# Kernel tuning notes

Measured on AMD Instinct MI355X. Metric: run time of the kernel, lower is better.

## Reference

```python
import jax, jax.numpy as jnp
import numpy as np

D_MODEL = 1024
NUM_HEADS = 16


def setup_inputs() -> dict:
    key = jax.random.key(0)
    ks = jax.random.split(key, 11)
    B, T, D = 4, 2048, D_MODEL
    scale = 1.0 / np.sqrt(D)
    inp = {
        'q': jax.random.normal(ks[0], (B, T, D), jnp.float32),
        'k': jax.random.normal(ks[1], (B, T, D), jnp.float32),
        'v': jax.random.normal(ks[2], (B, T, D), jnp.float32),
        'W_q': jax.random.normal(ks[3], (D, D), jnp.float32) * scale,
        'b_q': jnp.zeros((D,), jnp.float32),
        'W_k': jax.random.normal(ks[4], (D, D), jnp.float32) * scale,
        'b_k': jnp.zeros((D,), jnp.float32),
        'W_v': jax.random.normal(ks[5], (D, D), jnp.float32) * scale,
        'b_v': jnp.zeros((D,), jnp.float32),
        'W_o': jax.random.normal(ks[6], (D, D), jnp.float32) * scale,
        'b_o': jnp.zeros((D,), jnp.float32),
    }
    return inp


def reference(q, k, v, W_q, b_q, W_k, b_k, W_v, b_v, W_o, b_o):
    B, T, D = q.shape
    H = NUM_HEADS
    hd = D // H  # head dim

    def split_heads(x):  # [B,T,D] -> [B,H,T,hd]
        return x.reshape(B, T, H, hd).transpose(0, 2, 1, 3)

    qh = split_heads(q @ W_q + b_q)
    kh = split_heads(k @ W_k + b_k)
    vh = split_heads(v @ W_v + b_v)

    score = jnp.einsum('bhqd,bhkd->bhqk', qh, kh) / jnp.sqrt(jnp.float32(hd))
    attn = jax.nn.softmax(score, axis=-1)
    out = jnp.einsum('bhqk,bhkd->bhqd', attn, vh)  # [B,H,T,hd]
    out = out.transpose(0, 2, 1, 3).reshape(B, T, D)
    return out @ W_o + b_o
```

## Files before the change

kernel.cpp:

```cpp
#include <hip/hip_runtime.h>

typedef __attribute__((ext_vector_type(8))) short s8v;
typedef __attribute__((ext_vector_type(4))) float f4v;
typedef __attribute__((ext_vector_type(16))) float f16v;
typedef __attribute__((ext_vector_type(8))) unsigned short u8v;
typedef __attribute__((ext_vector_type(4))) unsigned short u16x4;
typedef __attribute__((ext_vector_type(4))) unsigned int uint4v;

#define B_ 4
#define T_ 2048
#define D_ 1024
#define H_ 16
#define HD_ 64

__device__ __forceinline__ unsigned short f2bf(float f) {
  unsigned int u = __builtin_bit_cast(unsigned int, f);
  u += 0x7fffu + ((u >> 16) & 1u);
  return (unsigned short)(u >> 16);
}

__device__ __forceinline__ unsigned int packbf2(float lo, float hi) {
  unsigned int u0 = __builtin_bit_cast(unsigned int, lo) + 0x8000u;
  unsigned int u1 = __builtin_bit_cast(unsigned int, hi) + 0x8000u;
  return __builtin_amdgcn_perm(u1, u0, 0x07060302u);
}

__device__ __forceinline__ void gload_lds16(const void* g, void* l) {
  __builtin_amdgcn_global_load_lds(
      (const __attribute__((address_space(1))) unsigned int*)g,
      (__attribute__((address_space(3))) unsigned int*)l, 16, 0, 0);
}

__global__ __launch_bounds__(256) void wt_cvt(
    const float* __restrict__ Wq, const float* __restrict__ Wk,
    const float* __restrict__ Wv, const float* __restrict__ Wo,
    unsigned short* __restrict__ Tq, unsigned short* __restrict__ Tk,
    unsigned short* __restrict__ Tv, unsigned short* __restrict__ To) {
  __shared__ unsigned short tile[32][33];
  int z = blockIdx.z;
  const float* W = (z == 0) ? Wq : (z == 1) ? Wk : (z == 2) ? Wv : Wo;
  unsigned short* Wt = (z == 0) ? Tq : (z == 1) ? Tk : (z == 2) ? Tv : To;
  int k0 = blockIdx.x * 32, n0 = blockIdx.y * 32;
  int t = threadIdx.x;
  int r = t >> 3, c = (t & 7) * 4;
  float4 v = *(const float4*)(W + (size_t)(k0 + r) * D_ + n0 + c);
  tile[r][c + 0] = f2bf(v.x);
  tile[r][c + 1] = f2bf(v.y);
  tile[r][c + 2] = f2bf(v.z);
  tile[r][c + 3] = f2bf(v.w);
  __syncthreads();
  u16x4 o;
  o[0] = tile[c + 0][r];
  o[1] = tile[c + 1][r];
  o[2] = tile[c + 2][r];
  o[3] = tile[c + 3][r];
  *(u16x4*)(Wt + (size_t)(n0 + r) * D_ + k0 + c) = o;
}

__global__ __launch_bounds__(256) void repack_k(const unsigned short* __restrict__ Kp,
                                                unsigned short* __restrict__ Kf) {
  unsigned int g = blockIdx.x * 256 + threadIdx.x;
  unsigned int bh = g >> 14;
  unsigned int r = g & 16383;
  unsigned int c32 = r >> 8;
  unsigned int ks = (r >> 6) & 3;
  unsigned int l2 = r & 63;
  unsigned int l = l2 >> 1, hh = l2 & 1;
  unsigned int b = bh >> 4, h = bh & 15;
  size_t row = (size_t)b * T_ + c32 * 32 + l;
  u8v v = *(const u8v*)(Kp + row * D_ + h * HD_ + ks * 16 + hh * 8);
  *(u8v*)(Kf + (size_t)g * 8) = v;
}

__global__ __launch_bounds__(256) void repack_v(const unsigned short* __restrict__ Vp,
                                                unsigned short* __restrict__ Vf) {
  __shared__ unsigned short tl[64][72];
  unsigned int c64 = blockIdx.x;
  unsigned int bh = blockIdx.y;
  unsigned int b = bh >> 4, h = bh & 15;
  int tid = threadIdx.x;
#pragma unroll
  for (int i = 0; i < 2; i++) {
    int s = i * 256 + tid;
    int row = s >> 3, cir = s & 7;
    u8v v = *(const u8v*)(Vp + ((size_t)(b * T_ + c64 * 64 + row)) * D_ + h * HD_ + cir * 8);
    *(u8v*)&tl[row][cir * 8] = v;
  }
  __syncthreads();
#pragma unroll
  for (int i = 0; i < 2; i++) {
    int s = i * 256 + tid;
    int mdkk = s >> 6;
    int l2 = s & 63;
    int l = l2 >> 1, hh = l2 & 1;
    int md = mdkk >> 2, kk = mdkk & 3;
    u8v o;
#pragma unroll
    for (int j = 0; j < 8; j++) o[j] = tl[kk * 16 + hh * 8 + j][md * 32 + l];
    *(u8v*)(Vf + ((size_t)(bh * 32 + c64) * 8 + mdkk) * 512 + l2 * 8) = o;
  }
}

struct GemmArgs {
  const void* A[3];
  const unsigned short* B[3];
  const float* bias[3];
  void* C[3];
};

template <bool AF32, bool OUTF32>
__global__ __launch_bounds__(256) void gemm128(GemmArgs args, int M, int N, int K) {
  __shared__ unsigned char smem[(AF32 ? 16384 : 8192) + 8192];
  unsigned char* AsB = smem;
  unsigned char* BsB = smem + (AF32 ? 16384 : 8192);
  int z = blockIdx.z;
  const float* Af = (const float*)args.A[z];
  const unsigned short* Ab = (const unsigned short*)args.A[z];
  const unsigned short* Bt = args.B[z];
  const float* bias = args.bias[z];
  int tid = threadIdx.x;
  int wave = tid >> 6, lane = tid & 63;
  int dl = lane & 15, quad = lane >> 4;
  int wm = (wave >> 1) * 64, wn = (wave & 1) * 64;
  size_t m0 = (size_t)blockIdx.y * 128, n0 = (size_t)blockIdx.x * 128;
  f4v acc[4][4] = {};

  for (int k0 = 0; k0 < K; k0 += 32) {
    if constexpr (AF32) {
#pragma unroll
      for (int i = 0; i < 4; i++) {
        int s = i * 256 + tid;
        int row = s >> 3, cs = s & 7, csrc = cs ^ (row & 7);
        gload_lds16(Af + (m0 + row) * K + k0 + csrc * 4, AsB + s * 16);
      }
    } else {
#pragma unroll
      for (int i = 0; i < 2; i++) {
        int s = i * 256 + tid;
        int row = s >> 2, cs = s & 3, csrc = cs ^ ((row >> 1) & 3);
        gload_lds16(Ab + (m0 + row) * K + k0 + csrc * 8, AsB + s * 16);
      }
    }
#pragma unroll
    for (int i = 0; i < 2; i++) {
      int s = i * 256 + tid;
      int row = s >> 2, cs = s & 3, csrc = cs ^ ((row >> 1) & 3);
      gload_lds16(Bt + (n0 + row) * K + k0 + csrc * 8, BsB + s * 16);
    }
    __syncthreads();
    s8v af[4], bf4[4];
#pragma unroll
    for (int i = 0; i < 4; i++) {
      int row = wm + i * 16 + dl;
      if constexpr (AF32) {
        const float* Ar = (const float*)AsB + row * 32;
        int f = row & 7;
        float4 lo = *(const float4*)(Ar + ((2 * quad) ^ f) * 4);
        float4 hi = *(const float4*)(Ar + ((2 * quad + 1) ^ f) * 4);
        uint4v p;
        p[0] = packbf2(lo.x, lo.y);
        p[1] = packbf2(lo.z, lo.w);
        p[2] = packbf2(hi.x, hi.y);
        p[3] = packbf2(hi.z, hi.w);
        af[i] = __builtin_bit_cast(s8v, p);
      } else {
        const unsigned short* Ar = (const unsigned short*)AsB + row * 32;
        af[i] = *(const s8v*)(Ar + (quad ^ ((row >> 1) & 3)) * 8);
      }
    }
#pragma unroll
    for (int i = 0; i < 4; i++) {
      int row = wn + i * 16 + dl;
      const unsigned short* Br = (const unsigned short*)BsB + row * 32;
      bf4[i] = *(const s8v*)(Br + (quad ^ ((row >> 1) & 3)) * 8);
    }
#pragma unroll
    for (int mi = 0; mi < 4; mi++)
#pragma unroll
      for (int ni = 0; ni < 4; ni++)
        acc[mi][ni] = __builtin_amdgcn_mfma_f32_16x16x32_bf16(af[mi], bf4[ni], acc[mi][ni], 0, 0, 0);
    __syncthreads();
  }

#pragma unroll
  for (int ni = 0; ni < 4; ni++) {
    size_t col = n0 + wn + ni * 16 + dl;
    float bv = bias[col];
#pragma unroll
    for (int mi = 0; mi < 4; mi++) {
#pragma unroll
      for (int r = 0; r < 4; r++) {
        size_t row = m0 + wm + mi * 16 + quad * 4 + r;
        float v = acc[mi][ni][r] + bv;
        if constexpr (OUTF32) ((float*)args.C[z])[row * N + col] = v;
        else ((unsigned short*)args.C[z])[row * N + col] = f2bf(v);
      }
    }
  }
}

__global__ __launch_bounds__(256) void attn(
    const unsigned short* __restrict__ Q, const unsigned short* __restrict__ Kf,
    const unsigned short* __restrict__ Vf, unsigned short* __restrict__ Ctx) {
  int tid = threadIdx.x;
  int wave = tid >> 6, lane = tid & 63;
  int l31 = lane & 31, hh = lane >> 5;
  int b = blockIdx.z, h = blockIdx.y;
  int bh = b * H_ + h;
  int qbase = blockIdx.x * 128 + wave * 32;
  const unsigned short* Qb = Q + ((size_t)(b * T_ + qbase + l31)) * D_ + h * HD_;
  const unsigned short* Kfb = Kf + (size_t)bh * (T_ * HD_);
  const unsigned short* Vfb = Vf + (size_t)bh * (T_ * HD_);
  int lc = (l31 * 2 + hh) * 8;

  s8v qf[4];
#pragma unroll
  for (int ks = 0; ks < 4; ks++) qf[ks] = *(const s8v*)(Qb + ks * 16 + 8 * hh);

  f16v zero = {};
  f16v oacc[2] = {zero, zero};
  float l = 0.f;
  const float sc = 0.18033688011112042f;

  s8v kf[2][2][4];
#pragma unroll
  for (int ms = 0; ms < 2; ms++)
#pragma unroll
    for (int ks = 0; ks < 4; ks++)
      kf[0][ms][ks] = *(const s8v*)(Kfb + (size_t)(ms * 4 + ks) * 512 + lc);

#pragma unroll 2
  for (int it = 0; it < T_ / 64; ++it) {
    int kt = it * 64;
    int cur = it & 1, nxt = cur ^ 1;
    s8v vf[2][4];
#pragma unroll
    for (int md = 0; md < 2; md++)
#pragma unroll
      for (int kk = 0; kk < 4; kk++)
        vf[md][kk] = *(const s8v*)(Vfb + ((size_t)(kt >> 6) * 8 + md * 4 + kk) * 512 + lc);
    int ktn = (kt + 64) & (T_ - 1);
#pragma unroll
    for (int ms = 0; ms < 2; ms++)
#pragma unroll
      for (int ks = 0; ks < 4; ks++)
        kf[nxt][ms][ks] = *(const s8v*)(Kfb + ((size_t)((ktn >> 5) + ms) * 4 + ks) * 512 + lc);

    f16v sacc[2] = {zero, zero};
#pragma unroll
    for (int ks = 0; ks < 4; ks++)
#pragma unroll
      for (int ms = 0; ms < 2; ms++)
        sacc[ms] = __builtin_amdgcn_mfma_f32_32x32x16_bf16(kf[cur][ms][ks], qf[ks], sacc[ms], 0, 0, 0);

    unsigned int pk[2][8];
#pragma unroll
    for (int ms = 0; ms < 2; ms++)
#pragma unroll
      for (int i = 0; i < 8; i++) {
        float p0 = exp2f(__builtin_fmaf(sacc[ms][2 * i], sc, -16.f));
        float p1 = exp2f(__builtin_fmaf(sacc[ms][2 * i + 1], sc, -16.f));
        l += p0 + p1;
        pk[ms][i] = packbf2(p0, p1);
      }

#pragma unroll
    for (int kk = 0; kk < 4; kk++) {
      int ms = kk >> 1, e4 = (kk & 1) * 4;
      unsigned int y0 = __shfl_xor(pk[ms][e4 + 2], 32);
      unsigned int y1 = __shfl_xor(pk[ms][e4 + 3], 32);
      unsigned int y2 = __shfl_xor(pk[ms][e4 + 0], 32);
      unsigned int y3 = __shfl_xor(pk[ms][e4 + 1], 32);
      uint4v pd;
      pd[0] = hh ? y0 : pk[ms][e4 + 0];
      pd[1] = hh ? y1 : pk[ms][e4 + 1];
      pd[2] = hh ? pk[ms][e4 + 2] : y2;
      pd[3] = hh ? pk[ms][e4 + 3] : y3;
      s8v pf = __builtin_bit_cast(s8v, pd);
#pragma unroll
      for (int md = 0; md < 2; md++)
        oacc[md] = __builtin_amdgcn_mfma_f32_32x32x16_bf16(vf[md][kk], pf, oacc[md], 0, 0, 0);
    }
  }

  l += __shfl_xor(l, 32);
  float inv = 1.0f / l;
  unsigned short* crow = Ctx + ((size_t)(b * T_ + qbase + l31)) * D_ + h * HD_;
#pragma unroll
  for (int md = 0; md < 2; md++)
#pragma unroll
    for (int hi = 0; hi < 4; hi++) {
      unsigned int w0 = packbf2(oacc[md][hi * 4 + 0] * inv, oacc[md][hi * 4 + 1] * inv);
      unsigned int w1 = packbf2(oacc[md][hi * 4 + 2] * inv, oacc[md][hi * 4 + 3] * inv);
      unsigned int* dst = (unsigned int*)(crow + md * 32 + hi * 8 + 4 * hh);
      dst[0] = w0;
      dst[1] = w1;
    }
}

extern "C" void kernel_launch(void* const* d_in, const int* in_sizes, int n_in,
                              void* d_out, int out_size, void* d_ws, size_t ws_size,
                              hipStream_t stream) {
  const float* q = (const float*)d_in[0];
  const float* k = (const float*)d_in[1];
  const float* v = (const float*)d_in[2];
  const float* Wq = (const float*)d_in[3];
  const float* bq = (const float*)d_in[4];
  const float* Wk = (const float*)d_in[5];
  const float* bk = (const float*)d_in[6];
  const float* Wv = (const float*)d_in[7];
  const float* bv = (const float*)d_in[8];
  const float* Wo = (const float*)d_in[9];
  const float* bo = (const float*)d_in[10];
  float* out = (float*)d_out;

  char* ws = (char*)d_ws;
  const size_t MB = 1ull << 20;
  unsigned short* Tq = (unsigned short*)(ws + 0 * MB);
  unsigned short* Tk = (unsigned short*)(ws + 2 * MB);
  unsigned short* Tv = (unsigned short*)(ws + 4 * MB);
  unsigned short* To = (unsigned short*)(ws + 6 * MB);
  unsigned short* Qp = (unsigned short*)(ws + 8 * MB);
  unsigned short* Kp = (unsigned short*)(ws + 24 * MB);
  unsigned short* Vp = (unsigned short*)(ws + 40 * MB);
  unsigned short* Kf = (unsigned short*)(ws + 56 * MB);
  unsigned short* Vf = (unsigned short*)(ws + 72 * MB);
  unsigned short* Ctx = Kp;
  const int M = B_ * T_;

  wt_cvt<<<dim3(32, 32, 4), 256, 0, stream>>>(Wq, Wk, Wv, Wo, Tq, Tk, Tv, To);

  GemmArgs ga;
  ga.A[0] = q;  ga.A[1] = k;  ga.A[2] = v;
  ga.B[0] = Tq; ga.B[1] = Tk; ga.B[2] = Tv;
  ga.bias[0] = bq; ga.bias[1] = bk; ga.bias[2] = bv;
  ga.C[0] = Qp; ga.C[1] = Kp; ga.C[2] = Vp;
  gemm128<true, false><<<dim3(D_ / 128, M / 128, 3), 256, 0, stream>>>(ga, M, D_, D_);

  repack_k<<<dim3(4096), 256, 0, stream>>>(Kp, Kf);
  repack_v<<<dim3(32, 64), 256, 0, stream>>>(Vp, Vf);

  attn<<<dim3(T_ / 128, H_, B_), 256, 0, stream>>>(Qp, Kf, Vf, Ctx);

  GemmArgs go;
  go.A[0] = Ctx; go.B[0] = To; go.bias[0] = bo; go.C[0] = out;
  gemm128<false, true><<<dim3(D_ / 128, M / 128, 1), 256, 0, stream>>>(go, M, D_, D_);
}
```

Before: 515.4 us.

## Reshape QKV GEMM wave tiling and remap attention blocks for XCD locality

The fp32-input QKV projection GEMM now gives each wave a 32x128 tile instead of 64x64. Each wave converts fewer fp32 A rows to bf16, in exchange for more B fragment loads per wave. The attention kernel now launches single-wave blocks on a flat grid of 4096. Block IDs are remapped so that all query blocks of one (batch, head) land on the same XCD, aiming for better L2 reuse of K/V. Smaller blocks may change occupancy and scheduling overhead.

```diff
diff --git a/kernel.cpp b/kernel.cpp
--- a/kernel.cpp
+++ b/kernel.cpp
@@ -110,6 +110,8 @@
 
 template <bool AF32, bool OUTF32>
 __global__ __launch_bounds__(256) void gemm128(GemmArgs args, int M, int N, int K) {
+  constexpr int MI = AF32 ? 2 : 4;
+  constexpr int NI = AF32 ? 8 : 4;
   __shared__ unsigned char smem[(AF32 ? 16384 : 8192) + 8192];
   unsigned char* AsB = smem;
   unsigned char* BsB = smem + (AF32 ? 16384 : 8192);
@@ -121,9 +123,10 @@
   int tid = threadIdx.x;
   int wave = tid >> 6, lane = tid & 63;
   int dl = lane & 15, quad = lane >> 4;
-  int wm = (wave >> 1) * 64, wn = (wave & 1) * 64;
+  int wm = AF32 ? wave * 32 : (wave >> 1) * 64;
+  int wn = AF32 ? 0 : (wave & 1) * 64;
   size_t m0 = (size_t)blockIdx.y * 128, n0 = (size_t)blockIdx.x * 128;
-  f4v acc[4][4] = {};
+  f4v acc[MI][NI] = {};
 
   for (int k0 = 0; k0 < K; k0 += 32) {
     if constexpr (AF32) {
@@ -148,9 +151,9 @@
       gload_lds16(Bt + (n0 + row) * K + k0 + csrc * 8, BsB + s * 16);
     }
     __syncthreads();
-    s8v af[4], bf4[4];
-#pragma unroll
-    for (int i = 0; i < 4; i++) {
+    s8v af[MI], bf4[NI];
+#pragma unroll
+    for (int i = 0; i < MI; i++) {
       int row = wm + i * 16 + dl;
       if constexpr (AF32) {
         const float* Ar = (const float*)AsB + row * 32;
@@ -169,25 +172,25 @@
       }
     }
 #pragma unroll
-    for (int i = 0; i < 4; i++) {
+    for (int i = 0; i < NI; i++) {
       int row = wn + i * 16 + dl;
       const unsigned short* Br = (const unsigned short*)BsB + row * 32;
       bf4[i] = *(const s8v*)(Br + (quad ^ ((row >> 1) & 3)) * 8);
     }
 #pragma unroll
-    for (int mi = 0; mi < 4; mi++)
-#pragma unroll
-      for (int ni = 0; ni < 4; ni++)
+    for (int mi = 0; mi < MI; mi++)
+#pragma unroll
+      for (int ni = 0; ni < NI; ni++)
         acc[mi][ni] = __builtin_amdgcn_mfma_f32_16x16x32_bf16(af[mi], bf4[ni], acc[mi][ni], 0, 0, 0);
     __syncthreads();
   }
 
 #pragma unroll
-  for (int ni = 0; ni < 4; ni++) {
+  for (int ni = 0; ni < NI; ni++) {
     size_t col = n0 + wn + ni * 16 + dl;
     float bv = bias[col];
 #pragma unroll
-    for (int mi = 0; mi < 4; mi++) {
+    for (int mi = 0; mi < MI; mi++) {
 #pragma unroll
       for (int r = 0; r < 4; r++) {
         size_t row = m0 + wm + mi * 16 + quad * 4 + r;
@@ -199,15 +202,17 @@
   }
 }
 
-__global__ __launch_bounds__(256) void attn(
+__global__ __launch_bounds__(64) void attn(
     const unsigned short* __restrict__ Q, const unsigned short* __restrict__ Kf,
     const unsigned short* __restrict__ Vf, unsigned short* __restrict__ Ctx) {
-  int tid = threadIdx.x;
-  int wave = tid >> 6, lane = tid & 63;
+  int bid = blockIdx.x;
+  int xcd = bid & 7, slot = bid >> 3;
+  int q32 = slot & 63;
+  int bh = (slot >> 6) * 8 + xcd;
+  int b = bh >> 4, h = bh & 15;
+  int lane = threadIdx.x;
   int l31 = lane & 31, hh = lane >> 5;
-  int b = blockIdx.z, h = blockIdx.y;
-  int bh = b * H_ + h;
-  int qbase = blockIdx.x * 128 + wave * 32;
+  int qbase = q32 * 32;
   const unsigned short* Qb = Q + ((size_t)(b * T_ + qbase + l31)) * D_ + h * HD_;
   const unsigned short* Kfb = Kf + (size_t)bh * (T_ * HD_);
   const unsigned short* Vfb = Vf + (size_t)bh * (T_ * HD_);
@@ -340,7 +345,7 @@
   repack_k<<<dim3(4096), 256, 0, stream>>>(Kp, Kf);
   repack_v<<<dim3(32, 64), 256, 0, stream>>>(Vp, Vf);
 
-  attn<<<dim3(T_ / 128, H_, B_), 256, 0, stream>>>(Qp, Kf, Vf, Ctx);
+  attn<<<dim3(4096), 64, 0, stream>>>(Qp, Kf, Vf, Ctx);
 
   GemmArgs go;
   go.A[0] = Ctx; go.B[0] = To; go.bias[0] = bo; go.C[0] = out;
```

Result: no change. 508.8 us (-1.3%).
